# Kernel optimization log

Hardware: AMD Instinct MI355X
Metric: run time of the kernel (lower is better)

The kernel has to match this reference:

```python
import jax, jax.numpy as jnp
import numpy as np


def setup_inputs() -> dict:
    key = jax.random.key(0)
    ks = jax.random.split(key, 5)
    B, N, H, S, D = 1, 256, 4, 256, 32
    q = jax.random.normal(ks[0], (B, N, H, S, D), dtype=jnp.float32)
    k = jax.random.normal(ks[1], (B, N, H, S, D), dtype=jnp.float32)
    v = jax.random.normal(ks[2], (B, N, H, S, D), dtype=jnp.float32)
    mask_bias = jax.random.normal(ks[3], (B, N, 1, 1, S), dtype=jnp.float32)
    triangle_bias = jax.random.normal(ks[4], (B, 1, H, S, S), dtype=jnp.float32)
    return {"q": q, "k": k, "v": v, "mask_bias": mask_bias, "triangle_bias": triangle_bias}


def reference(q, k, v, mask_bias, triangle_bias):
    # q,k,v: [B, N, H, S, D]; mask_bias: [B, N, 1, 1, S]; triangle_bias: [B, 1, H, S, S]
    D = q.shape[-1]
    sm_scale = 1.0 / jnp.sqrt(jnp.asarray(D, dtype=q.dtype))
    # scores: [B, N, H, S, S] (query index s attends over key index t)
    scores = jnp.einsum("bnhsd,bnhtd->bnhst", q, k) * sm_scale
    scores = scores + mask_bias + triangle_bias  # broadcast add of both biases
    p = jax.nn.softmax(scores, axis=-1)
    out = jnp.einsum("bnhst,bnhtd->bnhsd", p, v)
    return out
```

## Files before the change

### kernel.cpp

```cpp
#include <hip/hip_runtime.h>

typedef __bf16 bf16;
typedef bf16 bf16x2 __attribute__((ext_vector_type(2)));
typedef bf16 bf16x4 __attribute__((ext_vector_type(4)));
typedef bf16 bf16x8 __attribute__((ext_vector_type(8)));
typedef float f32x4 __attribute__((ext_vector_type(4)));
typedef float f32x16 __attribute__((ext_vector_type(16)));
typedef int i32x2 __attribute__((ext_vector_type(2)));
typedef int i32x4 __attribute__((ext_vector_type(4)));

#define SEQ 256
#define DH  32
#define VT_PAD 264

static __device__ __forceinline__ int pk2(float a, float b) {
    bf16x2 t; t[0] = (bf16)a; t[1] = (bf16)b;
    return __builtin_bit_cast(int, t);
}

static __device__ __forceinline__ bf16x8 cvt8(f32x4 a, f32x4 b) {
    bf16x8 f;
    f[0]=(bf16)a[0]; f[1]=(bf16)a[1]; f[2]=(bf16)a[2]; f[3]=(bf16)a[3];
    f[4]=(bf16)b[0]; f[5]=(bf16)b[1]; f[6]=(bf16)b[2]; f[7]=(bf16)b[3];
    return f;
}

template<int G>
static __device__ __forceinline__ i32x2 pgrp(f32x16 cf, f32x4 tg, f32x4 mk, float& lp) {
    constexpr float K1    = 0.17677669529663687f * 1.44269504088896f;
    constexpr float LOG2E = 1.44269504088896f;
    float p0 = __builtin_amdgcn_exp2f(fmaf(cf[4*G+0], K1, fmaf(tg[0], LOG2E, mk[0])));
    float p1 = __builtin_amdgcn_exp2f(fmaf(cf[4*G+1], K1, fmaf(tg[1], LOG2E, mk[1])));
    float p2 = __builtin_amdgcn_exp2f(fmaf(cf[4*G+2], K1, fmaf(tg[2], LOG2E, mk[2])));
    float p3 = __builtin_amdgcn_exp2f(fmaf(cf[4*G+3], K1, fmaf(tg[3], LOG2E, mk[3])));
    lp += (p0 + p1) + (p2 + p3);
    i32x2 r; r[0] = pk2(p0, p1); r[1] = pk2(p2, p3);
    return r;
}

static __device__ __forceinline__ void frags(i32x2 a0, i32x2 a1, i32x2 a2, i32x2 a3,
                                             bf16x8& f0, bf16x8& f1) {
    i32x2 s0 = __builtin_amdgcn_permlane32_swap(a0[0], a1[0], false, false);
    i32x2 s1 = __builtin_amdgcn_permlane32_swap(a0[1], a1[1], false, false);
    i32x2 s2 = __builtin_amdgcn_permlane32_swap(a2[0], a3[0], false, false);
    i32x2 s3 = __builtin_amdgcn_permlane32_swap(a2[1], a3[1], false, false);
    i32x4 w0 = {s0[0], s1[0], s0[1], s1[1]};
    i32x4 w1 = {s2[0], s3[0], s2[1], s3[1]};
    f0 = __builtin_bit_cast(bf16x8, w0);
    f1 = __builtin_bit_cast(bf16x8, w1);
}

__global__ __launch_bounds__(256, 2) void attn_mfma_kernel(
    const float* __restrict__ q,
    const float* __restrict__ k,
    const float* __restrict__ v,
    const float* __restrict__ mask_bias,
    const float* __restrict__ tri_bias,
    float* __restrict__ out)
{
    __shared__ bf16 Vt[DH][VT_PAD];
    __shared__ float Ml[SEQ];

    const int tid  = threadIdx.x;
    const int wave = tid >> 6;
    const int lane = tid & 63;
    const int l31  = lane & 31;
    const int hi   = lane >> 5;

    const int inst = blockIdx.x;
    const int n    = inst >> 2;
    const int h    = inst & 3;

    const float* qb = q + (size_t)inst * SEQ * DH;
    const float* kb = k + (size_t)inst * SEQ * DH;
    const float* vb = v + (size_t)inst * SEQ * DH;
    const float* mb = mask_bias + (size_t)n * SEQ;
    const float* tb = tri_bias + (size_t)h * SEQ * SEQ;

    constexpr float LOG2E = 1.44269504088896f;

    const int sbase = wave * 64;

    const float* trow0 = tb + (size_t)(sbase + l31) * SEQ + 4 * hi;
    const float* trow1 = trow0 + 32 * SEQ;

    const float* kp0 = kb + (size_t)l31 * DH + hi * 8;
    f32x4 kA = ((const f32x4*)kp0)[0];
    f32x4 kB = ((const f32x4*)kp0)[1];
    f32x4 kC = ((const f32x4*)(kp0 + 16))[0];
    f32x4 kD = ((const f32x4*)(kp0 + 16))[1];
    f32x4 tp0 = *(const f32x4*)(trow0 + 0);
    f32x4 tp1 = *(const f32x4*)(trow0 + 8);
    f32x4 tp2 = *(const f32x4*)(trow0 + 16);
    f32x4 tp3 = *(const f32x4*)(trow0 + 24);

    bf16x8 qf00, qf01, qf10, qf11;
    {
        const float* p0 = qb + (size_t)(sbase + l31) * DH + hi * 8;
        const float* p1 = qb + (size_t)(sbase + 32 + l31) * DH + hi * 8;
        qf00 = cvt8(((const f32x4*)p0)[0], ((const f32x4*)p0)[1]);
        qf01 = cvt8(((const f32x4*)(p0 + 16))[0], ((const f32x4*)(p0 + 16))[1]);
        qf10 = cvt8(((const f32x4*)p1)[0], ((const f32x4*)p1)[1]);
        qf11 = cvt8(((const f32x4*)(p1 + 16))[0], ((const f32x4*)(p1 + 16))[1]);
    }

    #pragma unroll
    for (int i = 0; i < 8; ++i) {
        int idx = i * 256 + tid;
        int t   = idx >> 3;
        int d4  = (idx & 7) * 4;
        f32x4 tv = ((const f32x4*)vb)[idx];
        Vt[d4 + 0][t] = (bf16)tv[0];
        Vt[d4 + 1][t] = (bf16)tv[1];
        Vt[d4 + 2][t] = (bf16)tv[2];
        Vt[d4 + 3][t] = (bf16)tv[3];
    }
    Ml[tid] = mb[tid] * LOG2E;
    __syncthreads();

    f32x16 oacc0 = {}, oacc1 = {};
    float lp0 = 0.f, lp1 = 0.f;
    const f32x16 z16 = {};

    for (int c = 0; c < 8; ++c) {
        const int tb0 = c * 32;

        bf16x8 kf0 = cvt8(kA, kB);
        bf16x8 kf1 = cvt8(kC, kD);
        f32x4 t0 = tp0, t1 = tp1, t2 = tp2, t3 = tp3;

        f32x4 u0 = *(const f32x4*)(trow1 + tb0 + 0);
        f32x4 u1 = *(const f32x4*)(trow1 + tb0 + 8);
        f32x4 u2 = *(const f32x4*)(trow1 + tb0 + 16);
        f32x4 u3 = *(const f32x4*)(trow1 + tb0 + 24);

        if (c < 7) {
            const float* kp = kb + (size_t)(tb0 + 32 + l31) * DH + hi * 8;
            kA = ((const f32x4*)kp)[0];
            kB = ((const f32x4*)kp)[1];
            kC = ((const f32x4*)(kp + 16))[0];
            kD = ((const f32x4*)(kp + 16))[1];
            tp0 = *(const f32x4*)(trow0 + tb0 + 32);
            tp1 = *(const f32x4*)(trow0 + tb0 + 40);
            tp2 = *(const f32x4*)(trow0 + tb0 + 48);
            tp3 = *(const f32x4*)(trow0 + tb0 + 56);
        }

        bf16x8 vf0 = *(const bf16x8*)&Vt[l31][tb0 + hi * 8];
        bf16x8 vf1 = *(const bf16x8*)&Vt[l31][tb0 + 16 + hi * 8];

        f32x4 mk0 = *(const f32x4*)&Ml[tb0 +  0 + 4 * hi];
        f32x4 mk1 = *(const f32x4*)&Ml[tb0 +  8 + 4 * hi];
        f32x4 mk2 = *(const f32x4*)&Ml[tb0 + 16 + 4 * hi];
        f32x4 mk3 = *(const f32x4*)&Ml[tb0 + 24 + 4 * hi];

        __builtin_amdgcn_s_setprio(1);
        f32x16 cf = __builtin_amdgcn_mfma_f32_32x32x16_bf16(kf0, qf00, z16, 0, 0, 0);
        cf = __builtin_amdgcn_mfma_f32_32x32x16_bf16(kf1, qf01, cf, 0, 0, 0);
        __builtin_amdgcn_s_setprio(0);

        i32x2 a0 = pgrp<0>(cf, t0, mk0, lp0);
        i32x2 a1 = pgrp<1>(cf, t1, mk1, lp0);
        i32x2 a2 = pgrp<2>(cf, t2, mk2, lp0);
        i32x2 a3 = pgrp<3>(cf, t3, mk3, lp0);
        bf16x8 pa0, pa1;
        frags(a0, a1, a2, a3, pa0, pa1);

        __builtin_amdgcn_s_setprio(1);
        oacc0 = __builtin_amdgcn_mfma_f32_32x32x16_bf16(pa0, vf0, oacc0, 0, 0, 0);
        oacc0 = __builtin_amdgcn_mfma_f32_32x32x16_bf16(pa1, vf1, oacc0, 0, 0, 0);

        cf = __builtin_amdgcn_mfma_f32_32x32x16_bf16(kf0, qf10, z16, 0, 0, 0);
        cf = __builtin_amdgcn_mfma_f32_32x32x16_bf16(kf1, qf11, cf, 0, 0, 0);
        __builtin_amdgcn_s_setprio(0);

        a0 = pgrp<0>(cf, u0, mk0, lp1);
        a1 = pgrp<1>(cf, u1, mk1, lp1);
        a2 = pgrp<2>(cf, u2, mk2, lp1);
        a3 = pgrp<3>(cf, u3, mk3, lp1);
        bf16x8 pb0, pb1;
        frags(a0, a1, a2, a3, pb0, pb1);

        __builtin_amdgcn_s_setprio(1);
        oacc1 = __builtin_amdgcn_mfma_f32_32x32x16_bf16(pb0, vf0, oacc1, 0, 0, 0);
        oacc1 = __builtin_amdgcn_mfma_f32_32x32x16_bf16(pb1, vf1, oacc1, 0, 0, 0);
        __builtin_amdgcn_s_setprio(0);
    }

    lp0 += __shfl_xor(lp0, 32);
    lp1 += __shfl_xor(lp1, 32);
    const float li0 = 1.0f / lp0;
    const float li1 = 1.0f / lp1;

    float* ob = out + (size_t)inst * SEQ * DH;
    #pragma unroll
    for (int r = 0; r < 16; ++r) {
        const int srow = (r & 3) + 8 * (r >> 2) + 4 * hi;
        float i0 = __shfl(li0, srow);
        float i1 = __shfl(li1, srow);
        ob[(size_t)(sbase + srow) * DH + l31]      = oacc0[r] * i0;
        ob[(size_t)(sbase + 32 + srow) * DH + l31] = oacc1[r] * i1;
    }
}

extern "C" void kernel_launch(void* const* d_in, const int* in_sizes, int n_in,
                              void* d_out, int out_size, void* d_ws, size_t ws_size,
                              hipStream_t stream) {
    const float* q    = (const float*)d_in[0];
    const float* k    = (const float*)d_in[1];
    const float* v    = (const float*)d_in[2];
    const float* mask = (const float*)d_in[3];
    const float* tri  = (const float*)d_in[4];
    float* out = (float*)d_out;

    attn_mfma_kernel<<<dim3(256 * 4), dim3(256), 0, stream>>>(q, k, v, mask, tri, out);
}
```

Baseline: 168.1 us.

## Stage K and triangle bias through LDS with coalesced prefetched loads

K is converted to bf16 once per block and stored in shared memory, so the four waves no longer each fetch and convert the full K from global memory. The triangle bias is read with row-contiguous coalesced loads into a per-wave LDS staging tile. Those loads are prefetched two chunks ahead in registers and stored mid-iteration, between the MFMA groups. This trades more LDS traffic and about 75KB of shared memory per block for fewer, better-coalesced global loads. The larger LDS footprint risks limiting occupancy.

```diff
diff --git a/kernel.cpp b/kernel.cpp
--- a/kernel.cpp
+++ b/kernel.cpp
@@ -12,6 +12,8 @@
 #define SEQ 256
 #define DH  32
 #define VT_PAD 264
+#define KB_PAD 40
+#define TRP 36
 
 static __device__ __forceinline__ int pk2(float a, float b) {
     bf16x2 t; t[0] = (bf16)a; t[1] = (bf16)b;
@@ -50,6 +52,26 @@
     f1 = __builtin_bit_cast(bf16x8, w1);
 }
 
+#define LOAD_TRI(cc)                                              \
+    sA = *(const f32x4*)(tstage + (cc) * 32 + 0 * 8 * SEQ);       \
+    sB = *(const f32x4*)(tstage + (cc) * 32 + 1 * 8 * SEQ);       \
+    sC = *(const f32x4*)(tstage + (cc) * 32 + 2 * 8 * SEQ);       \
+    sD = *(const f32x4*)(tstage + (cc) * 32 + 3 * 8 * SEQ);       \
+    sE = *(const f32x4*)(tstage + (cc) * 32 + 4 * 8 * SEQ);       \
+    sF = *(const f32x4*)(tstage + (cc) * 32 + 5 * 8 * SEQ);       \
+    sG = *(const f32x4*)(tstage + (cc) * 32 + 6 * 8 * SEQ);       \
+    sH = *(const f32x4*)(tstage + (cc) * 32 + 7 * 8 * SEQ);
+
+#define STORE_TRI()                                               \
+    *(f32x4*)(twr + 0 * 8 * TRP) = sA;                            \
+    *(f32x4*)(twr + 1 * 8 * TRP) = sB;                            \
+    *(f32x4*)(twr + 2 * 8 * TRP) = sC;                            \
+    *(f32x4*)(twr + 3 * 8 * TRP) = sD;                            \
+    *(f32x4*)(twr + 4 * 8 * TRP) = sE;                            \
+    *(f32x4*)(twr + 5 * 8 * TRP) = sF;                            \
+    *(f32x4*)(twr + 6 * 8 * TRP) = sG;                            \
+    *(f32x4*)(twr + 7 * 8 * TRP) = sH;
+
 __global__ __launch_bounds__(256, 2) void attn_mfma_kernel(
     const float* __restrict__ q,
     const float* __restrict__ k,
@@ -58,8 +80,10 @@
     const float* __restrict__ tri_bias,
     float* __restrict__ out)
 {
-    __shared__ bf16 Vt[DH][VT_PAD];
-    __shared__ float Ml[SEQ];
+    __shared__ __align__(16) bf16  Vt[DH][VT_PAD];
+    __shared__ __align__(16) bf16  Kb[SEQ][KB_PAD];
+    __shared__ __align__(16) float Ml[SEQ];
+    __shared__ __align__(16) float Tr[4][64][TRP];
 
     const int tid  = threadIdx.x;
     const int wave = tid >> 6;
@@ -81,18 +105,12 @@
 
     const int sbase = wave * 64;
 
-    const float* trow0 = tb + (size_t)(sbase + l31) * SEQ + 4 * hi;
-    const float* trow1 = trow0 + 32 * SEQ;
-
-    const float* kp0 = kb + (size_t)l31 * DH + hi * 8;
-    f32x4 kA = ((const f32x4*)kp0)[0];
-    f32x4 kB = ((const f32x4*)kp0)[1];
-    f32x4 kC = ((const f32x4*)(kp0 + 16))[0];
-    f32x4 kD = ((const f32x4*)(kp0 + 16))[1];
-    f32x4 tp0 = *(const f32x4*)(trow0 + 0);
-    f32x4 tp1 = *(const f32x4*)(trow0 + 8);
-    f32x4 tp2 = *(const f32x4*)(trow0 + 16);
-    f32x4 tp3 = *(const f32x4*)(trow0 + 24);
+    const float* tstage = tb + (size_t)(sbase + (lane >> 3)) * SEQ + (lane & 7) * 4;
+    float*       twr    = &Tr[wave][lane >> 3][(lane & 7) * 4];
+
+    f32x4 sA, sB, sC, sD, sE, sF, sG, sH;
+
+    LOAD_TRI(0);
 
     bf16x8 qf00, qf01, qf10, qf11;
     {
@@ -114,8 +132,16 @@
         Vt[d4 + 1][t] = (bf16)tv[1];
         Vt[d4 + 2][t] = (bf16)tv[2];
         Vt[d4 + 3][t] = (bf16)tv[3];
+        f32x4 tk = ((const f32x4*)kb)[idx];
+        bf16x4 kk;
+        kk[0]=(bf16)tk[0]; kk[1]=(bf16)tk[1]; kk[2]=(bf16)tk[2]; kk[3]=(bf16)tk[3];
+        *(bf16x4*)&Kb[t][d4] = kk;
     }
     Ml[tid] = mb[tid] * LOG2E;
+
+    STORE_TRI();
+    LOAD_TRI(1);
+
     __syncthreads();
 
     f32x16 oacc0 = {}, oacc1 = {};
@@ -125,27 +151,18 @@
     for (int c = 0; c < 8; ++c) {
         const int tb0 = c * 32;
 
-        bf16x8 kf0 = cvt8(kA, kB);
-        bf16x8 kf1 = cvt8(kC, kD);
-        f32x4 t0 = tp0, t1 = tp1, t2 = tp2, t3 = tp3;
-
-        f32x4 u0 = *(const f32x4*)(trow1 + tb0 + 0);
-        f32x4 u1 = *(const f32x4*)(trow1 + tb0 + 8);
-        f32x4 u2 = *(const f32x4*)(trow1 + tb0 + 16);
-        f32x4 u3 = *(const f32x4*)(trow1 + tb0 + 24);
-
-        if (c < 7) {
-            const float* kp = kb + (size_t)(tb0 + 32 + l31) * DH + hi * 8;
-            kA = ((const f32x4*)kp)[0];
-            kB = ((const f32x4*)kp)[1];
-            kC = ((const f32x4*)(kp + 16))[0];
-            kD = ((const f32x4*)(kp + 16))[1];
-            tp0 = *(const f32x4*)(trow0 + tb0 + 32);
-            tp1 = *(const f32x4*)(trow0 + tb0 + 40);
-            tp2 = *(const f32x4*)(trow0 + tb0 + 48);
-            tp3 = *(const f32x4*)(trow0 + tb0 + 56);
-        }
-
+        const float* trd = &Tr[wave][l31][hi * 4];
+        f32x4 t0 = *(const f32x4*)(trd + 0);
+        f32x4 t1 = *(const f32x4*)(trd + 8);
+        f32x4 t2 = *(const f32x4*)(trd + 16);
+        f32x4 t3 = *(const f32x4*)(trd + 24);
+        f32x4 u0 = *(const f32x4*)(trd + 32 * TRP + 0);
+        f32x4 u1 = *(const f32x4*)(trd + 32 * TRP + 8);
+        f32x4 u2 = *(const f32x4*)(trd + 32 * TRP + 16);
+        f32x4 u3 = *(const f32x4*)(trd + 32 * TRP + 24);
+
+        bf16x8 kf0 = *(const bf16x8*)&Kb[tb0 + l31][hi * 8];
+        bf16x8 kf1 = *(const bf16x8*)&Kb[tb0 + l31][16 + hi * 8];
         bf16x8 vf0 = *(const bf16x8*)&Vt[l31][tb0 + hi * 8];
         bf16x8 vf1 = *(const bf16x8*)&Vt[l31][tb0 + 16 + hi * 8];
 
@@ -169,7 +186,12 @@
         __builtin_amdgcn_s_setprio(1);
         oacc0 = __builtin_amdgcn_mfma_f32_32x32x16_bf16(pa0, vf0, oacc0, 0, 0, 0);
         oacc0 = __builtin_amdgcn_mfma_f32_32x32x16_bf16(pa1, vf1, oacc0, 0, 0, 0);
-
+        __builtin_amdgcn_s_setprio(0);
+
+        if (c < 7) { STORE_TRI(); }
+        if (c < 6) { LOAD_TRI(c + 2); }
+
+        __builtin_amdgcn_s_setprio(1);
         cf = __builtin_amdgcn_mfma_f32_32x32x16_bf16(kf0, qf10, z16, 0, 0, 0);
         cf = __builtin_amdgcn_mfma_f32_32x32x16_bf16(kf1, qf11, cf, 0, 0, 0);
         __builtin_amdgcn_s_setprio(0);
```

New measurement: 151.4 us. 1.11x faster.
